# Kernel optimization log

Hardware: AMD Instinct MI355X
Metric: run time of the kernel (lower is better)

The kernel has to match this reference:

```python
import jax, jax.numpy as jnp
import numpy as np

B, T = 64, 128
IN, H, L, OUT = 512, 1024, 2, 1


def _gru_scan(seq, Wi, Wh, bi, bh):
    # seq: (S, in_dim); PyTorch GRU cell, gate order r, z, n.
    h0 = jnp.zeros((H,), dtype=seq.dtype)
    def step(h, x):
        gi = x @ Wi.T + bi          # (3H,)
        gh = h @ Wh.T + bh          # (3H,)
        r = jax.nn.sigmoid(gi[:H] + gh[:H])
        z = jax.nn.sigmoid(gi[H:2 * H] + gh[H:2 * H])
        n = jnp.tanh(gi[2 * H:] + r * gh[2 * H:])
        h_new = (1.0 - z) * n + z * h
        return h_new, h_new
    _, hs = jax.lax.scan(step, h0, seq)
    return hs                        # (S, H)


def setup_inputs() -> dict:
    key = jax.random.key(0)
    ks = jax.random.split(key, 24)
    mk = lambda k, shape: jax.random.normal(k, shape, dtype=jnp.float32) * 0.05
    d = {}
    d['x'] = jax.random.normal(ks[0], (B, T, IN), dtype=jnp.float32)
    # gru1: layer0 input=IN, layer1 input=H
    d['g1_Wi0'] = mk(ks[1], (3 * H, IN)); d['g1_Wh0'] = mk(ks[2], (3 * H, H))
    d['g1_bi0'] = mk(ks[3], (3 * H,));    d['g1_bh0'] = mk(ks[4], (3 * H,))
    d['g1_Wi1'] = mk(ks[5], (3 * H, H));  d['g1_Wh1'] = mk(ks[6], (3 * H, H))
    d['g1_bi1'] = mk(ks[7], (3 * H,));    d['g1_bh1'] = mk(ks[8], (3 * H,))
    # gru2: both layers input=H
    d['g2_Wi0'] = mk(ks[9], (3 * H, H));  d['g2_Wh0'] = mk(ks[10], (3 * H, H))
    d['g2_bi0'] = mk(ks[11], (3 * H,));   d['g2_bh0'] = mk(ks[12], (3 * H,))
    d['g2_Wi1'] = mk(ks[13], (3 * H, H)); d['g2_Wh1'] = mk(ks[14], (3 * H, H))
    d['g2_bi1'] = mk(ks[15], (3 * H,));   d['g2_bh1'] = mk(ks[16], (3 * H,))
    d['fc1_W'] = mk(ks[17], (64, H));     d['fc1_b'] = mk(ks[18], (64,))
    d['fc2_W'] = mk(ks[19], (OUT, 64));   d['fc2_b'] = mk(ks[20], (OUT,))
    return d


def reference(x, g1_Wi0, g1_Wh0, g1_bi0, g1_bh0, g1_Wi1, g1_Wh1, g1_bi1, g1_bh1,
              g2_Wi0, g2_Wh0, g2_bi0, g2_bh0, g2_Wi1, g2_Wh1, g2_bi1, g2_bh1,
              fc1_W, fc1_b, fc2_W, fc2_b):
    # PyTorch feeds x[:, t, :] (2-D) to a batch_first GRU -> treated as an
    # UNBATCHED sequence of length B; hidden is carried across t. That equals
    # one GRU scan over the flattened (T*B)-step sequence, t-major / b-minor.
    seq = jnp.swapaxes(x, 0, 1).reshape(T * B, IN)
    hs0 = _gru_scan(seq, g1_Wi0, g1_Wh0, g1_bi0, g1_bh0)    # (T*B, H) layer 0
    hs1 = _gru_scan(hs0, g1_Wi1, g1_Wh1, g1_bi1, g1_bh1)    # (T*B, H) layer 1
    # h returned after timestep t is the hidden at flat step t*B + (B-1)
    s = jnp.stack([hs0, hs1], axis=1)[B - 1::B]             # (T, L, H)
    seq2 = s.reshape(T * L, H)                              # torch.cat(s)
    # gru2 over the [1, T*L, H] sequence (batch=1)
    hs2_0 = _gru_scan(seq2, g2_Wi0, g2_Wh0, g2_bi0, g2_bh0)
    hs2_1 = _gru_scan(hs2_0, g2_Wi1, g2_Wh1, g2_bi1, g2_bh1)
    h2 = jnp.stack([hs2_0[-1], hs2_1[-1]], axis=0)[:, None, :]  # (L, 1, H)
    y = jax.nn.sigmoid(h2 @ fc1_W.T + fc1_b)                # (L, 1, 64)
    out = jax.nn.sigmoid(y @ fc2_W.T + fc2_b)               # (L, 1, OUT)
    return out
```

## Files before the change

kernel.cpp:

```cpp
#include <hip/hip_runtime.h>


typedef unsigned u32x4 __attribute__((ext_vector_type(4)));
typedef unsigned u32x2 __attribute__((ext_vector_type(2)));
typedef _Float16 h2_t  __attribute__((ext_vector_type(2)));

#define NWG 256

__device__ u32x4    g_recL0[2][NWG];
__device__ u32x4    g_recL1[2][NWG];
__device__ unsigned g_seq2[256][512];

__device__ __forceinline__ unsigned pk(float a, float b) {
  unsigned short ua = __builtin_bit_cast(unsigned short, (_Float16)a);
  unsigned short ub = __builtin_bit_cast(unsigned short, (_Float16)b);
  return (unsigned)ua | ((unsigned)ub << 16);
}
__device__ __forceinline__ float unpk(unsigned u, int hi) {
  unsigned short us = (unsigned short)(hi ? (u >> 16) : (u & 0xffffu));
  return (float)__builtin_bit_cast(_Float16, us);
}

#if __has_builtin(__builtin_amdgcn_fdot2)
__device__ __forceinline__ float fdot2(unsigned a, unsigned b, float c) {
  return __builtin_amdgcn_fdot2(__builtin_bit_cast(h2_t, a),
                                __builtin_bit_cast(h2_t, b), c, false);
}
#else
__device__ __forceinline__ float fdot2(unsigned a, unsigned b, float c) {
  h2_t ha = __builtin_bit_cast(h2_t, a), hb = __builtin_bit_cast(h2_t, b);
  return c + (float)ha[0] * (float)hb[0] + (float)ha[1] * (float)hb[1];
}
#endif

__device__ __forceinline__ u32x4 ld_sc_v4(const u32x4* p) {
  u32x4 v;
  asm volatile("global_load_dwordx4 %0, %1, off sc1\n\t"
               "s_waitcnt vmcnt(0)"
               : "=&v"(v) : "v"(p) : "memory");
  return v;
}
__device__ __forceinline__ void ld_sc_2x4(const u32x4* p0, const u32x4* p1,
                                          u32x4& a, u32x4& b) {
  asm volatile("global_load_dwordx4 %0, %2, off sc1\n\t"
               "global_load_dwordx4 %1, %3, off sc1\n\t"
               "s_waitcnt vmcnt(0)"
               : "=&v"(a), "=&v"(b) : "v"(p0), "v"(p1) : "memory");
}
__device__ __forceinline__ void st_sc_v4(u32x4* p, u32x4 v) {
  asm volatile("global_store_dwordx4 %0, %1, off sc1"
               :: "v"(p), "v"(v) : "memory");
}
__device__ __forceinline__ void st_sc_v2(void* p, u32x2 v) {
  asm volatile("global_store_dwordx2 %0, %1, off sc1"
               :: "v"(p), "v"(v) : "memory");
}

__device__ __forceinline__ float sigf(float x) { return 1.f / (1.f + __expf(-x)); }

__device__ __forceinline__ int swzH_pos(int idx) {
  int ch = idx >> 2;
  ch ^= (ch >> 3) & 7;
  return (ch << 2) | (idx & 3);
}
__device__ __forceinline__ int swzX_pos(int idx) {
  int ch = idx >> 2;
  ch ^= (ch >> 2) & 7;
  return (ch << 2) | (idx & 3);
}

__global__ void init_recs() {
  int t = blockIdx.x * blockDim.x + threadIdx.x;
  u32x4 ff = {0u, 0u, 0xFFFFFFFFu, 0u};
  if (t < 512)       g_recL0[t >> 8][t & 255] = ff;
  else               g_recL1[(t - 512) >> 8][t & 255] = ff;
}

template <int PHASE>
__global__ __launch_bounds__(256, 1) void gru_phase(
    const float* __restrict__ Wm0, const float* __restrict__ Wm1,
    const float* __restrict__ Wm2, const float* __restrict__ Wm3,
    const float* __restrict__ bh0, const float* __restrict__ bi1,
    const float* __restrict__ bh1, const float* __restrict__ bi0,
    const float* __restrict__ x,
    const float* __restrict__ fc1W, const float* __restrict__ fc1b,
    const float* __restrict__ fc2W, const float* __restrict__ fc2b,
    float* __restrict__ out)
{
  constexpr int N0 = (PHASE == 1) ? 8192 : 256;
  constexpr int XC = (PHASE == 1) ? 512 : 1024;

  const int wg   = blockIdx.x;
  const int tid  = threadIdx.x;
  const int wave = tid >> 6;
  const int lane = tid & 63;
  const int g4   = lane >> 4;
  const int q    = lane & 15;
  const int j0   = wg * 4;

  __shared__ __attribute__((aligned(16))) unsigned sH0[2][512];
  __shared__ __attribute__((aligned(16))) unsigned sH1[2][512];
  __shared__ __attribute__((aligned(16))) unsigned sX [2][512];
  __shared__ float sD[2][48];
  __shared__ float sY[128];

  unsigned wreg[96];
  {
    const float* Wm = (wave == 0) ? Wm0 : (wave == 1) ? Wm1
                    : (wave == 2) ? Wm2 : Wm3;
    #pragma unroll
    for (int t = 0; t < 3; ++t) {
      const int rr = g4 * 3 + t;
      const int R  = (rr >> 2) * 1024 + j0 + (rr & 3);
      if (PHASE == 1 && wave == 3) {
        const float2* rp = (const float2*)(Wm + (size_t)R * XC + 32 * q);
        #pragma unroll
        for (int p = 0; p < 16; ++p) { float2 v = rp[p]; wreg[t*32 + p] = pk(v.x, v.y); }
      } else {
        const float2* rp = (const float2*)(Wm + (size_t)R * ((wave == 3) ? XC : 1024) + 64 * q);
        #pragma unroll
        for (int p = 0; p < 32; ++p) { float2 v = rp[p]; wreg[t*32 + p] = pk(v.x, v.y); }
      }
    }
  }

  float bI[3], bH[3];
  {
    const int i = lane & 3, layer = (lane >> 2) & 1;
    const float* pbi = layer ? bi1 : bi0;
    const float* pbh = layer ? bh1 : bh0;
    #pragma unroll
    for (int g = 0; g < 3; ++g) {
      bI[g] = pbi[g * 1024 + j0 + i];
      bH[g] = pbh[g * 1024 + j0 + i];
    }
  }

  for (int s = 0; s <= N0; ++s) {
    const int par = s & 1;

    float2 xv = {0.f, 0.f};
    unsigned xs0 = 0, xs1 = 0;
    if (PHASE == 1) {
      if (s < N0) {
        const int b = s & 63, tt = s >> 6;
        xv = ((const float2*)(x + (size_t)(b * 128 + tt) * 512))[tid];
      }
    } else {
      if (s < N0) { xs0 = g_seq2[s][2 * tid]; xs1 = g_seq2[s][2 * tid + 1]; }
    }

    unsigned d00 = 0, d01 = 0, d10 = 0, d11 = 0;
    if (s > 0) {
      const unsigned want = (unsigned)(s - 1);
      const u32x4* a0 = &g_recL0[(s - 1) & 1][tid];
      const u32x4* a1 = &g_recL1[(s - 1) & 1][tid];
      u32x4 r0, r1;
      ld_sc_2x4(a0, a1, r0, r1);
      while (r0[2] != want || r1[2] != want) {
        __builtin_amdgcn_s_sleep(1);
        ld_sc_2x4(a0, a1, r0, r1);
      }
      d00 = r0[0]; d01 = r0[1]; d10 = r1[0]; d11 = r1[1];
    }
    sH0[par][swzH_pos(2 * tid)]     = d00;
    sH0[par][swzH_pos(2 * tid + 1)] = d01;
    sH1[par][swzH_pos(2 * tid)]     = d10;
    sH1[par][swzH_pos(2 * tid + 1)] = d11;
    if (PHASE == 1) {
      if (s < N0) sX[par][swzX_pos(tid)] = pk(xv.x, xv.y);
    } else {
      if (s < N0) {
        sX[par][swzH_pos(2 * tid)]     = xs0;
        sX[par][swzH_pos(2 * tid + 1)] = xs1;
      }
    }
    __syncthreads();

    float acc0 = 0.f, acc1 = 0.f, acc2 = 0.f;
    if (PHASE == 1 && wave == 3) {
      const u32x4* Xv = (const u32x4*)sX[par];
      #pragma unroll
      for (int k = 0; k < 4; ++k) {
        u32x4 h4 = Xv[(4 * q + k) ^ (q & 7)];
        #pragma unroll
        for (int u = 0; u < 4; ++u) {
          const int p = 4 * k + u;
          acc0 = fdot2(wreg[p],      h4[u], acc0);
          acc1 = fdot2(wreg[32 + p], h4[u], acc1);
          acc2 = fdot2(wreg[64 + p], h4[u], acc2);
        }
      }
    } else {
      const unsigned* hb = (wave == 2) ? sH1[par] : (wave == 3) ? sX[par] : sH0[par];
      const u32x4* Hv = (const u32x4*)hb;
      #pragma unroll
      for (int k = 0; k < 8; ++k) {
        u32x4 h4 = Hv[8 * q + (k ^ (q & 7))];
        #pragma unroll
        for (int u = 0; u < 4; ++u) {
          const int p = 4 * k + u;
          acc0 = fdot2(wreg[p],      h4[u], acc0);
          acc1 = fdot2(wreg[32 + p], h4[u], acc1);
          acc2 = fdot2(wreg[64 + p], h4[u], acc2);
        }
      }
    }
    acc0 += __shfl_xor(acc0, 8, 16); acc0 += __shfl_xor(acc0, 4, 16);
    acc0 += __shfl_xor(acc0, 2, 16); acc0 += __shfl_xor(acc0, 1, 16);
    acc1 += __shfl_xor(acc1, 8, 16); acc1 += __shfl_xor(acc1, 4, 16);
    acc1 += __shfl_xor(acc1, 2, 16); acc1 += __shfl_xor(acc1, 1, 16);
    acc2 += __shfl_xor(acc2, 8, 16); acc2 += __shfl_xor(acc2, 4, 16);
    acc2 += __shfl_xor(acc2, 2, 16); acc2 += __shfl_xor(acc2, 1, 16);
    if (q < 3) {
      const float dv = (q == 0) ? acc0 : (q == 1) ? acc1 : acc2;
      sD[par][wave * 12 + g4 * 3 + q] = dv;
    }
    __syncthreads();

    if (wave == 0) {
      const int i = lane & 3;
      const int layer = (lane >> 2) & 1;
      const float* Sd = sD[par];
      const int mI = layer ? 12 : 36;
      const int mH = layer ? 24 : 0;
      const float pr  = Sd[mI + 0 + i] + bI[0] + Sd[mH + 0 + i] + bH[0];
      const float pz  = Sd[mI + 4 + i] + bI[1] + Sd[mH + 4 + i] + bH[1];
      const float gin = Sd[mI + 8 + i] + bI[2];
      const float ghn = Sd[mH + 8 + i] + bH[2];
      const float rg = sigf(pr), zg = sigf(pz);
      const float ng = tanhf(gin + rg * ghn);
      const int   jj = 2 * wg + (i >> 1);
      const unsigned hu = (layer ? sH1 : sH0)[par][swzH_pos(jj)];
      const float hp = unpk(hu, i & 1);
      float hn = (1.f - zg) * ng + zg * hp;
      const bool valid = layer ? (s >= 1) : (s < N0);
      hn = valid ? hn : 0.f;
      const float v0 = __shfl(hn, 0), v1 = __shfl(hn, 1);
      const float v2 = __shfl(hn, 2), v3 = __shfl(hn, 3);
      const float w0 = __shfl(hn, 4), w1 = __shfl(hn, 5);
      const float w2 = __shfl(hn, 6), w3 = __shfl(hn, 7);
      if (lane == 0) {
        u32x4 rec0 = {pk(v0, v1), pk(v2, v3), (unsigned)s, 0u};
        u32x4 rec1 = {pk(w0, w1), pk(w2, w3), (unsigned)s, 0u};
        st_sc_v4(&g_recL0[par][wg], rec0);
        st_sc_v4(&g_recL1[par][wg], rec1);
        if (PHASE == 1) {
          if ((s & 63) == 63) {
            u32x2 t2 = {rec0[0], rec0[1]};
            st_sc_v2(&g_seq2[2 * (s >> 6)][2 * wg], t2);
          }
          if (s >= 1 && ((s - 1) & 63) == 63) {
            u32x2 t2 = {rec1[0], rec1[1]};
            st_sc_v2(&g_seq2[2 * ((s - 1) >> 6) + 1][2 * wg], t2);
          }
        }
      }
    }
  }

  if (PHASE == 2 && wg == 0) {
    {
      const u32x4* a1 = &g_recL1[0][tid];
      u32x4 r1 = ld_sc_v4(a1);
      while (r1[2] != 256u) { __builtin_amdgcn_s_sleep(1); r1 = ld_sc_v4(a1); }
      sH1[0][swzH_pos(2 * tid)]     = r1[0];
      sH1[0][swzH_pos(2 * tid + 1)] = r1[1];
    }
    __syncthreads();
    if (tid < 128) {
      const int lsel = tid >> 6;
      const int k = tid & 63;
      const unsigned* Hs = lsel ? sH1[0] : sH0[0];
      const float* wrow = fc1W + (size_t)k * 1024;
      float a = fc1b[k];
      for (int j2 = 0; j2 < 512; ++j2) {
        const unsigned hu = Hs[swzH_pos(j2)];
        a += unpk(hu, 0) * wrow[2 * j2] + unpk(hu, 1) * wrow[2 * j2 + 1];
      }
      sY[tid] = sigf(a);
    }
    __syncthreads();
    if (tid < 2) {
      const float* yv = sY + tid * 64;
      float a = fc2b[0];
      for (int k2 = 0; k2 < 64; ++k2) a += fc2W[k2] * yv[k2];
      out[tid] = sigf(a);
    }
  }
}

extern "C" void kernel_launch(void* const* d_in, const int* in_sizes, int n_in,
                              void* d_out, int out_size, void* d_ws, size_t ws_size,
                              hipStream_t stream) {
  (void)in_sizes; (void)n_in; (void)out_size; (void)d_ws; (void)ws_size;
  const float* x      = (const float*)d_in[0];
  const float* g1_Wi0 = (const float*)d_in[1];
  const float* g1_Wh0 = (const float*)d_in[2];
  const float* g1_bi0 = (const float*)d_in[3];
  const float* g1_bh0 = (const float*)d_in[4];
  const float* g1_Wi1 = (const float*)d_in[5];
  const float* g1_Wh1 = (const float*)d_in[6];
  const float* g1_bi1 = (const float*)d_in[7];
  const float* g1_bh1 = (const float*)d_in[8];
  const float* g2_Wi0 = (const float*)d_in[9];
  const float* g2_Wh0 = (const float*)d_in[10];
  const float* g2_bi0 = (const float*)d_in[11];
  const float* g2_bh0 = (const float*)d_in[12];
  const float* g2_Wi1 = (const float*)d_in[13];
  const float* g2_Wh1 = (const float*)d_in[14];
  const float* g2_bi1 = (const float*)d_in[15];
  const float* g2_bh1 = (const float*)d_in[16];
  const float* fc1W   = (const float*)d_in[17];
  const float* fc1b   = (const float*)d_in[18];
  const float* fc2W   = (const float*)d_in[19];
  const float* fc2b   = (const float*)d_in[20];
  float* out = (float*)d_out;

  init_recs<<<dim3(4), dim3(256), 0, stream>>>();
  gru_phase<1><<<dim3(NWG), dim3(256), 0, stream>>>(
      g1_Wh0, g1_Wi1, g1_Wh1, g1_Wi0, g1_bh0, g1_bi1, g1_bh1, g1_bi0,
      x, fc1W, fc1b, fc2W, fc2b, out);
  gru_phase<2><<<dim3(NWG), dim3(256), 0, stream>>>(
      g2_Wh0, g2_Wi1, g2_Wh1, g2_Wi0, g2_bh0, g2_bi1, g2_bh1, g2_bi0,
      x, fc1W, fc1b, fc2W, fc2b, out);
}
```

Measured before the change: 29.04 ms.

## Split each GRU matvec across two waves along K with 512-thread blocks

Doubles the workgroup to 8 waves, so each of the four matrix roles is handled by two waves that each cover half of the reduction dimension. This halves the per-wave weight registers and the dot-product chain length, and the partial sums are combined in the gate-update stage. It also spreads the spin-wait loads over twice as many threads (one record per thread), and swaps the sigmoid and tanh for versions built on a fast reciprocal. The cost is larger blocks to synchronise at each barrier, more shared-memory partials to combine, and slightly lower precision in the activations.

Result: faster. 26.79 ms (-7.7%).

```diff
diff --git a/kernel.cpp b/kernel.cpp
--- a/kernel.cpp
+++ b/kernel.cpp
@@ -40,13 +40,6 @@
                : "=&v"(v) : "v"(p) : "memory");
   return v;
 }
-__device__ __forceinline__ void ld_sc_2x4(const u32x4* p0, const u32x4* p1,
-                                          u32x4& a, u32x4& b) {
-  asm volatile("global_load_dwordx4 %0, %2, off sc1\n\t"
-               "global_load_dwordx4 %1, %3, off sc1\n\t"
-               "s_waitcnt vmcnt(0)"
-               : "=&v"(a), "=&v"(b) : "v"(p0), "v"(p1) : "memory");
-}
 __device__ __forceinline__ void st_sc_v4(u32x4* p, u32x4 v) {
   asm volatile("global_store_dwordx4 %0, %1, off sc1"
                :: "v"(p), "v"(v) : "memory");
@@ -56,18 +49,26 @@
                :: "v"(p), "v"(v) : "memory");
 }
 
-__device__ __forceinline__ float sigf(float x) { return 1.f / (1.f + __expf(-x)); }
-
-__device__ __forceinline__ int swzH_pos(int idx) {
-  int ch = idx >> 2;
-  ch ^= (ch >> 3) & 7;
-  return (ch << 2) | (idx & 3);
-}
-__device__ __forceinline__ int swzX_pos(int idx) {
-  int ch = idx >> 2;
-  ch ^= (ch >> 2) & 7;
-  return (ch << 2) | (idx & 3);
-}
+__device__ __forceinline__ float rcpf(float x) {
+#if __has_builtin(__builtin_amdgcn_rcpf)
+  return __builtin_amdgcn_rcpf(x);
+#else
+  return 1.f / x;
+#endif
+}
+__device__ __forceinline__ float sigf(float x) {
+  return rcpf(1.f + __expf(-x));
+}
+__device__ __forceinline__ float tanh_f(float x) {
+  x = fminf(fmaxf(x, -15.f), 15.f);
+  const float e = __expf(2.f * x);
+  return (e - 1.f) * rcpf(e + 1.f);
+}
+
+__device__ __forceinline__ int swzHc(int ch) { return ch ^ ((ch >> 3) & 7); }
+__device__ __forceinline__ int swzXc(int ch) { return ch ^ ((ch >> 2) & 7); }
+__device__ __forceinline__ int swzH_pos(int idx) { return (swzHc(idx >> 2) << 2) | (idx & 3); }
+__device__ __forceinline__ int swzX_pos(int idx) { return (swzXc(idx >> 2) << 2) | (idx & 3); }
 
 __global__ void init_recs() {
   int t = blockIdx.x * blockDim.x + threadIdx.x;
@@ -77,7 +78,7 @@
 }
 
 template <int PHASE>
-__global__ __launch_bounds__(256, 1) void gru_phase(
+__global__ __launch_bounds__(512, 2) void gru_phase(
     const float* __restrict__ Wm0, const float* __restrict__ Wm1,
     const float* __restrict__ Wm2, const float* __restrict__ Wm3,
     const float* __restrict__ bh0, const float* __restrict__ bi1,
@@ -92,34 +93,36 @@
 
   const int wg   = blockIdx.x;
   const int tid  = threadIdx.x;
-  const int wave = tid >> 6;
+  const int wv   = tid >> 6;
   const int lane = tid & 63;
+  const int m    = wv >> 1;
+  const int kh   = wv & 1;
   const int g4   = lane >> 4;
   const int q    = lane & 15;
   const int j0   = wg * 4;
+  const bool m3s = (PHASE == 1) && (m == 3);
 
   __shared__ __attribute__((aligned(16))) unsigned sH0[2][512];
   __shared__ __attribute__((aligned(16))) unsigned sH1[2][512];
   __shared__ __attribute__((aligned(16))) unsigned sX [2][512];
-  __shared__ float sD[2][48];
+  __shared__ float sD[2][96];
   __shared__ float sY[128];
 
-  unsigned wreg[96];
+  unsigned wreg[48];
   {
-    const float* Wm = (wave == 0) ? Wm0 : (wave == 1) ? Wm1
-                    : (wave == 2) ? Wm2 : Wm3;
+    const float* Wm = (m == 0) ? Wm0 : (m == 1) ? Wm1 : (m == 2) ? Wm2 : Wm3;
+    const int cols = (m == 3) ? XC : 1024;
     #pragma unroll
     for (int t = 0; t < 3; ++t) {
       const int rr = g4 * 3 + t;
       const int R  = (rr >> 2) * 1024 + j0 + (rr & 3);
-      if (PHASE == 1 && wave == 3) {
-        const float2* rp = (const float2*)(Wm + (size_t)R * XC + 32 * q);
+      const float2* rp = (const float2*)(Wm + (size_t)R * cols + kh * (cols / 2) + q * (cols / 32));
+      if (m3s) {
         #pragma unroll
-        for (int p = 0; p < 16; ++p) { float2 v = rp[p]; wreg[t*32 + p] = pk(v.x, v.y); }
+        for (int p = 0; p < 8; ++p)  { float2 v = rp[p]; wreg[t * 8 + p]  = pk(v.x, v.y); }
       } else {
-        const float2* rp = (const float2*)(Wm + (size_t)R * ((wave == 3) ? XC : 1024) + 64 * q);
         #pragma unroll
-        for (int p = 0; p < 32; ++p) { float2 v = rp[p]; wreg[t*32 + p] = pk(v.x, v.y); }
+        for (int p = 0; p < 16; ++p) { float2 v = rp[p]; wreg[t * 16 + p] = pk(v.x, v.y); }
       }
     }
   }
@@ -140,69 +143,67 @@
     const int par = s & 1;
 
     float2 xv = {0.f, 0.f};
-    unsigned xs0 = 0, xs1 = 0;
+    unsigned xs = 0;
     if (PHASE == 1) {
-      if (s < N0) {
+      if (s < N0 && tid < 256) {
         const int b = s & 63, tt = s >> 6;
         xv = ((const float2*)(x + (size_t)(b * 128 + tt) * 512))[tid];
       }
     } else {
-      if (s < N0) { xs0 = g_seq2[s][2 * tid]; xs1 = g_seq2[s][2 * tid + 1]; }
-    }
-
-    unsigned d00 = 0, d01 = 0, d10 = 0, d11 = 0;
-    if (s > 0) {
-      const unsigned want = (unsigned)(s - 1);
-      const u32x4* a0 = &g_recL0[(s - 1) & 1][tid];
-      const u32x4* a1 = &g_recL1[(s - 1) & 1][tid];
-      u32x4 r0, r1;
-      ld_sc_2x4(a0, a1, r0, r1);
-      while (r0[2] != want || r1[2] != want) {
-        __builtin_amdgcn_s_sleep(1);
-        ld_sc_2x4(a0, a1, r0, r1);
-      }
-      d00 = r0[0]; d01 = r0[1]; d10 = r1[0]; d11 = r1[1];
-    }
-    sH0[par][swzH_pos(2 * tid)]     = d00;
-    sH0[par][swzH_pos(2 * tid + 1)] = d01;
-    sH1[par][swzH_pos(2 * tid)]     = d10;
-    sH1[par][swzH_pos(2 * tid + 1)] = d11;
+      if (s < N0) xs = g_seq2[s][tid];
+    }
+
+    const int t2 = tid & 255;
+    {
+      unsigned d0 = 0, d1 = 0;
+      if (s > 0) {
+        const unsigned want = (unsigned)(s - 1);
+        const u32x4* a = (tid < 256) ? &g_recL0[(s - 1) & 1][t2]
+                                     : &g_recL1[(s - 1) & 1][t2];
+        u32x4 r = ld_sc_v4(a);
+        while (r[2] != want) {
+          __builtin_amdgcn_s_sleep(1);
+          r = ld_sc_v4(a);
+        }
+        d0 = r[0]; d1 = r[1];
+      }
+      unsigned* dst = (tid < 256) ? sH0[par] : sH1[par];
+      dst[swzH_pos(2 * t2)]     = d0;
+      dst[swzH_pos(2 * t2 + 1)] = d1;
+    }
     if (PHASE == 1) {
-      if (s < N0) sX[par][swzX_pos(tid)] = pk(xv.x, xv.y);
+      if (s < N0 && tid < 256) sX[par][swzX_pos(tid)] = pk(xv.x, xv.y);
     } else {
-      if (s < N0) {
-        sX[par][swzH_pos(2 * tid)]     = xs0;
-        sX[par][swzH_pos(2 * tid + 1)] = xs1;
-      }
+      if (s < N0) sX[par][swzH_pos(tid)] = xs;
     }
     __syncthreads();
 
     float acc0 = 0.f, acc1 = 0.f, acc2 = 0.f;
-    if (PHASE == 1 && wave == 3) {
+    if (m3s) {
       const u32x4* Xv = (const u32x4*)sX[par];
       #pragma unroll
-      for (int k = 0; k < 4; ++k) {
-        u32x4 h4 = Xv[(4 * q + k) ^ (q & 7)];
+      for (int k = 0; k < 2; ++k) {
+        u32x4 h4 = Xv[swzXc(kh * 32 + 2 * q + k)];
         #pragma unroll
         for (int u = 0; u < 4; ++u) {
           const int p = 4 * k + u;
           acc0 = fdot2(wreg[p],      h4[u], acc0);
-          acc1 = fdot2(wreg[32 + p], h4[u], acc1);
-          acc2 = fdot2(wreg[64 + p], h4[u], acc2);
+          acc1 = fdot2(wreg[8 + p],  h4[u], acc1);
+          acc2 = fdot2(wreg[16 + p], h4[u], acc2);
         }
       }
     } else {
-      const unsigned* hb = (wave == 2) ? sH1[par] : (wave == 3) ? sX[par] : sH0[par];
+      const unsigned* hb = (m == 2) ? sH1[par] : (m == 3) ? sX[par] : sH0[par];
       const u32x4* Hv = (const u32x4*)hb;
       #pragma unroll
-      for (int k = 0; k < 8; ++k) {
-        u32x4 h4 = Hv[8 * q + (k ^ (q & 7))];
+      for (int k = 0; k < 4; ++k) {
+        u32x4 h4 = Hv[swzHc(kh * 64 + 4 * q + k)];
         #pragma unroll
         for (int u = 0; u < 4; ++u) {
           const int p = 4 * k + u;
           acc0 = fdot2(wreg[p],      h4[u], acc0);
-          acc1 = fdot2(wreg[32 + p], h4[u], acc1);
-          acc2 = fdot2(wreg[64 + p], h4[u], acc2);
+          acc1 = fdot2(wreg[16 + p], h4[u], acc1);
+          acc2 = fdot2(wreg[32 + p], h4[u], acc2);
         }
       }
     }
@@ -214,22 +215,25 @@
     acc2 += __shfl_xor(acc2, 2, 16); acc2 += __shfl_xor(acc2, 1, 16);
     if (q < 3) {
       const float dv = (q == 0) ? acc0 : (q == 1) ? acc1 : acc2;
-      sD[par][wave * 12 + g4 * 3 + q] = dv;
+      sD[par][m * 24 + kh * 12 + g4 * 3 + q] = dv;
     }
     __syncthreads();
 
-    if (wave == 0) {
+    if (wv == 0) {
       const int i = lane & 3;
       const int layer = (lane >> 2) & 1;
       const float* Sd = sD[par];
-      const int mI = layer ? 12 : 36;
-      const int mH = layer ? 24 : 0;
-      const float pr  = Sd[mI + 0 + i] + bI[0] + Sd[mH + 0 + i] + bH[0];
-      const float pz  = Sd[mI + 4 + i] + bI[1] + Sd[mH + 4 + i] + bH[1];
-      const float gin = Sd[mI + 8 + i] + bI[2];
-      const float ghn = Sd[mH + 8 + i] + bH[2];
-      const float rg = sigf(pr), zg = sigf(pz);
-      const float ng = tanhf(gin + rg * ghn);
+      const int mI = layer ? 1 : 3;
+      const int mH = layer ? 2 : 0;
+      const float dIr = Sd[mI * 24 + 0 + i] + Sd[mI * 24 + 12 + 0 + i];
+      const float dIz = Sd[mI * 24 + 4 + i] + Sd[mI * 24 + 12 + 4 + i];
+      const float dIn = Sd[mI * 24 + 8 + i] + Sd[mI * 24 + 12 + 8 + i];
+      const float dHr = Sd[mH * 24 + 0 + i] + Sd[mH * 24 + 12 + 0 + i];
+      const float dHz = Sd[mH * 24 + 4 + i] + Sd[mH * 24 + 12 + 4 + i];
+      const float dHn = Sd[mH * 24 + 8 + i] + Sd[mH * 24 + 12 + 8 + i];
+      const float rg = sigf(dIr + bI[0] + dHr + bH[0]);
+      const float zg = sigf(dIz + bI[1] + dHz + bH[1]);
+      const float ng = tanh_f(dIn + bI[2] + rg * (dHn + bH[2]));
       const int   jj = 2 * wg + (i >> 1);
       const unsigned hu = (layer ? sH1 : sH0)[par][swzH_pos(jj)];
       const float hp = unpk(hu, i & 1);
@@ -247,12 +251,12 @@
         st_sc_v4(&g_recL1[par][wg], rec1);
         if (PHASE == 1) {
           if ((s & 63) == 63) {
-            u32x2 t2 = {rec0[0], rec0[1]};
-            st_sc_v2(&g_seq2[2 * (s >> 6)][2 * wg], t2);
+            u32x2 t2v = {rec0[0], rec0[1]};
+            st_sc_v2(&g_seq2[2 * (s >> 6)][2 * wg], t2v);
           }
           if (s >= 1 && ((s - 1) & 63) == 63) {
-            u32x2 t2 = {rec1[0], rec1[1]};
-            st_sc_v2(&g_seq2[2 * ((s - 1) >> 6) + 1][2 * wg], t2);
+            u32x2 t2v = {rec1[0], rec1[1]};
+            st_sc_v2(&g_seq2[2 * ((s - 1) >> 6) + 1][2 * wg], t2v);
           }
         }
       }
@@ -260,7 +264,7 @@
   }
 
   if (PHASE == 2 && wg == 0) {
-    {
+    if (tid < 256) {
       const u32x4* a1 = &g_recL1[0][tid];
       u32x4 r1 = ld_sc_v4(a1);
       while (r1[2] != 256u) { __builtin_amdgcn_s_sleep(1); r1 = ld_sc_v4(a1); }
@@ -318,10 +322,10 @@
   float* out = (float*)d_out;
 
   init_recs<<<dim3(4), dim3(256), 0, stream>>>();
-  gru_phase<1><<<dim3(NWG), dim3(256), 0, stream>>>(
+  gru_phase<1><<<dim3(NWG), dim3(512), 0, stream>>>(
       g1_Wh0, g1_Wi1, g1_Wh1, g1_Wi0, g1_bh0, g1_bi1, g1_bh1, g1_bi0,
       x, fc1W, fc1b, fc2W, fc2b, out);
-  gru_phase<2><<<dim3(NWG), dim3(256), 0, stream>>>(
+  gru_phase<2><<<dim3(NWG), dim3(512), 0, stream>>>(
       g2_Wh0, g2_Wi1, g2_Wh1, g2_Wi0, g2_bh0, g2_bi1, g2_bh1, g2_bi0,
       x, fc1W, fc1b, fc2W, fc2b, out);
 }
```
